# Kernel optimization log

Measured on AMD Instinct MI355X. Metric: run time of the kernel, lower is better.

Reference implementation:

```python
import jax, jax.numpy as jnp
import numpy as np

D_MODEL, D_STATE, EXPAND = 1024, 16, 2
D_INNER = EXPAND * D_MODEL
BATCH, SEQ = 4, 4096


def setup_inputs() -> dict:
    key = jax.random.key(0)
    ks = jax.random.split(key, 9)
    s = 0.02
    return {
        "x": jax.random.normal(ks[0], (BATCH, SEQ, D_MODEL), jnp.float32),
        # torch Linear weight [out,in] stored transposed here as [in,out]
        "W_in": jax.random.normal(ks[1], (D_MODEL, 2 * D_INNER), jnp.float32) * s,
        "conv_w": jax.random.normal(ks[2], (D_INNER, 1, 3), jnp.float32) * s,  # depthwise, groups=D_INNER
        "conv_b": jax.random.normal(ks[3], (D_INNER,), jnp.float32) * s,
        "W_B": jax.random.normal(ks[4], (D_INNER, D_STATE), jnp.float32) * s,
        "W_C": jax.random.normal(ks[5], (D_INNER, D_STATE), jnp.float32) * s,
        "A": jax.random.normal(ks[6], (D_STATE,), jnp.float32),
        "D": jnp.ones((D_INNER,), jnp.float32),
        "W_out": jax.random.normal(ks[7], (D_INNER, D_MODEL), jnp.float32) * s,
    }


def reference(x, W_in, conv_w, conv_b, W_B, W_C, A, D, W_out):
    d_inner = conv_w.shape[0]
    # input projection and split into main / residual gate paths
    xr = jnp.einsum("bld,de->ble", x, W_in)  # [B, L, 2*d_inner]
    x_main, res = xr[..., :d_inner], xr[..., d_inner:]
    # depthwise conv1d along seq (kernel 3, pad 1)
    xc = jax.lax.conv_general_dilated(
        x_main.transpose(0, 2, 1), conv_w, (1,), [(1, 1)],
        dimension_numbers=("NCH", "OIH", "NCH"), feature_group_count=d_inner)
    xc = (xc + conv_b[None, :, None]).transpose(0, 2, 1)  # [B, L, d_inner]
    xc = jax.nn.silu(xc)
    # selective-scan inputs
    Bt = jnp.einsum("bli,is->bls", xc, W_B)  # [B, L, d_state]
    Ct = jnp.einsum("bli,is->bls", xc, W_C)
    decay = jnp.exp(-jax.nn.softplus(A))  # exp(A_diag), [d_state]

    def step(state, bc):
        b_t, c_t = bc
        state = state * decay + b_t  # i=0: zeros*decay + B[0] == B[0]
        return state, jnp.sum(state * c_t, axis=-1)  # scalar per batch

    _, ys = jax.lax.scan(step, jnp.zeros_like(Bt[:, 0]),
                         (Bt.transpose(1, 0, 2), Ct.transpose(1, 0, 2)))
    ys = ys.T  # [B, L]
    y = ys[..., None] + xc * D  # broadcast scan output across d_inner
    y = y * jax.nn.silu(res)
    return jnp.einsum("bli,id->bld", y, W_out)
```

## Files before the change

### kernel.cpp

```cpp
#include <hip/hip_runtime.h>


typedef _Float16 half8 __attribute__((ext_vector_type(8)));
typedef float floatx4 __attribute__((ext_vector_type(4)));

#define D_MODEL 1024
#define D_INNER 2048
#define SEQ     4096
#define NBATCH  4
#define NROWS   (NBATCH * SEQ)
#define CHUNK   16
#define NCHUNK  (SEQ / CHUNK)
#define NTASK   (NBATCH * NCHUNK)

__device__ __forceinline__ void async16(_Float16* lds, const _Float16* g) {
    __builtin_amdgcn_global_load_lds((const __attribute__((address_space(1))) void*)g,
                                     (__attribute__((address_space(3))) void*)lds, 16, 0, 0);
}

__device__ __forceinline__ float siluf(float x) {
    return x / (1.f + __expf(-x));
}

__device__ __forceinline__ float decay_of(const float* A, int s) {
    return __expf(-log1pf(__expf(A[s])));
}


__global__ __launch_bounds__(256) void convert_f32_f16(const float* __restrict__ src,
                                                       _Float16* __restrict__ dst) {
    size_t idx = ((size_t)blockIdx.x * 256 + threadIdx.x) * 8;
    float4 a = *(const float4*)(src + idx);
    float4 b = *(const float4*)(src + idx + 4);
    half8 o = {(_Float16)a.x, (_Float16)a.y, (_Float16)a.z, (_Float16)a.w,
               (_Float16)b.x, (_Float16)b.y, (_Float16)b.z, (_Float16)b.w};
    *(half8*)(dst + idx) = o;
}

__global__ __launch_bounds__(256) void transpose_to_f16(const float* __restrict__ src,
                                                        _Float16* __restrict__ dst,
                                                        int K, int N) {
    __shared__ float tile[32][33];
    int n0 = blockIdx.x * 32, k0 = blockIdx.y * 32;
    int x = threadIdx.x, y = threadIdx.y;
#pragma unroll
    for (int r = 0; r < 32; r += 8)
        tile[y + r][x] = src[(size_t)(k0 + y + r) * N + (n0 + x)];
    __syncthreads();
#pragma unroll
    for (int r = 0; r < 32; r += 8)
        dst[(size_t)(n0 + y + r) * K + (k0 + x)] = (_Float16)tile[x][y + r];
}

__global__ __launch_bounds__(256) void convert_wbct(const float* __restrict__ WB,
                                                    const float* __restrict__ WC,
                                                    _Float16* __restrict__ WBCT) {
    int idx = blockIdx.x * 256 + threadIdx.x;
    int n = idx >> 11, k = idx & 2047;
    float v = (n < 16) ? WB[k * 16 + n] : WC[k * 16 + (n - 16)];
    WBCT[idx] = (_Float16)v;
}


__device__ __forceinline__ void stage_half(const _Float16* __restrict__ src, int K,
                                           int rowBase, int k0, _Float16* ldsHalf) {
    const int tid = threadIdx.x;
    const int sr = tid >> 3, wid = tid >> 6;
    const int lc = ((tid & 7) ^ (sr & 7)) << 3;
#pragma unroll
    for (int r = 0; r < 2; r++) {
        const _Float16* g = src + (size_t)(rowBase + r * 64 + sr) * K + (k0 + lc);
        async16(ldsHalf + r * 4096 + wid * 512, g);
    }
}

#define GP_LOAD(MQ, NQ, LOADA)                                                          \
    if (LOADA) {                                                                        \
        _Pragma("unroll") for (int m = 0; m < 4; m++) {                                 \
            const int lr = (MQ) * 128 + wm * 64 + m * 16 + fr;                          \
            _Pragma("unroll") for (int s = 0; s < 2; s++)                               \
                af[m][s] = *(const half8*)(Ab + lr * 64 + ((((s << 2) + q) ^ frq) << 3)); \
        }                                                                               \
    }                                                                                   \
    {                                                                                   \
        _Pragma("unroll") for (int n = 0; n < 2; n++) {                                 \
            const int br = (NQ) * 128 + wn * 32 + n * 16 + fr;                          \
            _Pragma("unroll") for (int s = 0; s < 2; s++)                               \
                bf[n][s] = *(const half8*)(Bb + br * 64 + ((((s << 2) + q) ^ frq) << 3)); \
        }                                                                               \
    }

#define GP_MMA(MQ, NQ)                                                                  \
    __builtin_amdgcn_s_barrier();                                                       \
    asm volatile("s_waitcnt lgkmcnt(0)" ::: "memory");                                  \
    __builtin_amdgcn_s_setprio(1);                                                      \
    _Pragma("unroll") for (int m = 0; m < 4; m++)                                       \
        _Pragma("unroll") for (int n = 0; n < 2; n++)                                   \
            _Pragma("unroll") for (int s = 0; s < 2; s++)                               \
                acc[(MQ) * 4 + m][(NQ) * 2 + n] = __builtin_amdgcn_mfma_f32_16x16x32_f16( \
                    af[m][s], bf[n][s], acc[(MQ) * 4 + m][(NQ) * 2 + n], 0, 0, 0);      \
    __builtin_amdgcn_s_setprio(0);                                                      \
    __builtin_amdgcn_s_barrier();

template <typename OutT>
__global__ __launch_bounds__(512, 2) void gemm256(const _Float16* __restrict__ A,
                                                  const _Float16* __restrict__ BT,
                                                  OutT* __restrict__ C,
                                                  int M, int N, int K) {
    __shared__ __align__(16) _Float16 smem[4 * 16384];
    _Float16* const AsBase = smem;
    _Float16* const BsBase = smem + 32768;

    const int tid = threadIdx.x;
    const int wid = tid >> 6, lane = tid & 63;
    const int wm = wid >> 2, wn = wid & 3;
    const int fr = lane & 15, q = lane >> 4, frq = fr & 7;

    int lin = blockIdx.y * gridDim.x + blockIdx.x;
    const int nwg = gridDim.x * gridDim.y;
    lin = (lin & 7) * (nwg >> 3) + (lin >> 3);
    const int bx = lin % gridDim.x, by = lin / gridDim.x;
    const int row0 = by * 256, col0 = bx * 256;
    const int NT = K >> 6;

    floatx4 acc[8][4] = {};
    half8 af[4][2], bf[2][2];

    stage_half(A,  K, row0,       0, AsBase);
    stage_half(BT, K, col0,       0, BsBase);
    stage_half(A,  K, row0 + 128, 0, AsBase + 8192);
    stage_half(BT, K, col0 + 128, 0, BsBase + 8192);
    if (NT > 1) {
        stage_half(A,  K, row0, 64, AsBase + 16384);
        stage_half(BT, K, col0, 64, BsBase + 16384);
        asm volatile("s_waitcnt vmcnt(4)" ::: "memory");
    } else {
        asm volatile("s_waitcnt vmcnt(0)" ::: "memory");
    }
    __builtin_amdgcn_s_barrier();

    for (int t = 0; t < NT; ++t) {
        _Float16* Ab  = AsBase + ((t & 1) << 14);
        _Float16* Bb  = BsBase + ((t & 1) << 14);
        _Float16* Abn = AsBase + (((t + 1) & 1) << 14);
        _Float16* Bbn = BsBase + (((t + 1) & 1) << 14);
        const int k1 = (t + 1) << 6, k2 = (t + 2) << 6;
        const bool s1 = (t + 1) < NT, s2 = (t + 2) < NT;

        GP_LOAD(0, 0, 1);
        if (s1) stage_half(A, K, row0 + 128, k1, Abn + 8192);
        GP_MMA(0, 0);

        GP_LOAD(0, 1, 0);
        if (s1) stage_half(BT, K, col0 + 128, k1, Bbn + 8192);
        GP_MMA(0, 1);

        GP_LOAD(1, 0, 1);
        if (s2) stage_half(A, K, row0, k2, Ab);
        GP_MMA(1, 0);

        GP_LOAD(1, 1, 0);
        if (s2) stage_half(BT, K, col0, k2, Bb);
        if (s2) {
            asm volatile("s_waitcnt vmcnt(4)" ::: "memory");
        } else if (t + 2 == NT) {
            asm volatile("s_waitcnt vmcnt(0)" ::: "memory");
        }
        GP_MMA(1, 1);
    }

    const int er = (lane >> 4) * 4, ec = lane & 15;
#pragma unroll
    for (int fi = 0; fi < 8; fi++)
#pragma unroll
        for (int fj = 0; fj < 4; fj++)
#pragma unroll
            for (int r = 0; r < 4; r++) {
                int row = row0 + (fi >> 2) * 128 + wm * 64 + (fi & 3) * 16 + er + r;
                int col = col0 + (fj >> 1) * 128 + wn * 32 + (fj & 1) * 16 + ec;
                C[(size_t)row * N + col] = (OutT)acc[fi][fj][r];
            }
}

__global__ __launch_bounds__(256) void conv_bc_fin(const _Float16* __restrict__ xr,
                                                   const float* __restrict__ cw,
                                                   const float* __restrict__ cb,
                                                   const _Float16* __restrict__ WBCT,
                                                   const float* __restrict__ A,
                                                   _Float16* __restrict__ xc,
                                                   float* __restrict__ BtCt,
                                                   float* __restrict__ fin) {
    __shared__ __align__(16) _Float16 As[4 * 32 * 128];
    const int tid = threadIdx.x, wid = tid >> 6, lane = tid & 63;
    const int row0 = blockIdx.x * 32;
    const int l0 = row0 & (SEQ - 1);
    const int cg = lane & 15;
    const int rg = lane >> 4;
    const int fr = lane & 15, q = lane >> 4;
    _Float16* As_w = As + wid * 4096;
    const int r0 = rg * 8;

    floatx4 acc[2][2] = {};

    for (int t = 0; t < 4; t++) {
        const int kbase = wid * 512 + t * 128;
        const int gcol = kbase + cg * 8;
        float w0[8], w1[8], w2[8], bb[8];
#pragma unroll
        for (int j = 0; j < 8; j++) {
            w0[j] = cw[(gcol + j) * 3];
            w1[j] = cw[(gcol + j) * 3 + 1];
            w2[j] = cw[(gcol + j) * 3 + 2];
            bb[j] = cb[gcol + j];
        }
        half8 prev = {}, cur, nxt;
        if (!(l0 == 0 && rg == 0))
            prev = *(const half8*)(xr + (size_t)(row0 + r0 - 1) * 4096 + gcol);
        cur = *(const half8*)(xr + (size_t)(row0 + r0) * 4096 + gcol);
#pragma unroll
        for (int r = 0; r < 8; r++) {
            if (r == 7 && rg == 3 && l0 + 32 == SEQ) {
                half8 z = {};
                nxt = z;
            } else {
                nxt = *(const half8*)(xr + (size_t)(row0 + r0 + r + 1) * 4096 + gcol);
            }
            half8 o;
#pragma unroll
            for (int j = 0; j < 8; j++) {
                float a = (float)prev[j] * w0[j] + (float)cur[j] * w1[j] +
                          (float)nxt[j] * w2[j] + bb[j];
                o[j] = (_Float16)siluf(a);
            }
            const int lrow = r0 + r;
            *(half8*)(xc + (size_t)(row0 + lrow) * D_INNER + gcol) = o;
            *(half8*)(As_w + lrow * 128 + ((cg ^ (lrow & 7)) * 8)) = o;
            prev = cur;
            cur = nxt;
        }
#pragma unroll
        for (int ks = 0; ks < 4; ks++) {
            half8 af[2], bf[2];
#pragma unroll
            for (int rt = 0; rt < 2; rt++)
                af[rt] = *(const half8*)(As_w + (rt * 16 + fr) * 128 +
                                         (((ks * 4 + q) ^ (fr & 7)) * 8));
#pragma unroll
            for (int ot = 0; ot < 2; ot++)
                bf[ot] = *(const half8*)(WBCT + (size_t)(ot * 16 + fr) * D_INNER +
                                         kbase + ks * 32 + q * 8);
#pragma unroll
            for (int rt = 0; rt < 2; rt++)
#pragma unroll
                for (int ot = 0; ot < 2; ot++)
                    acc[rt][ot] = __builtin_amdgcn_mfma_f32_16x16x32_f16(af[rt], bf[ot], acc[rt][ot], 0, 0, 0);
        }
    }

    __syncthreads();
    float* red = (float*)As;
    float* btl = (float*)As + 4096;
    const int er = (lane >> 4) * 4, ec = lane & 15;
#pragma unroll
    for (int rt = 0; rt < 2; rt++)
#pragma unroll
        for (int ot = 0; ot < 2; ot++)
#pragma unroll
            for (int rr = 0; rr < 4; rr++)
                red[wid * 1024 + (rt * 16 + er + rr) * 32 + ot * 16 + ec] = acc[rt][ot][rr];
    __syncthreads();
#pragma unroll
    for (int i = 0; i < 4; i++) {
        int idx = i * 256 + tid;
        float v = red[idx] + red[1024 + idx] + red[2048 + idx] + red[3072 + idx];
        btl[idx] = v;
        BtCt[(size_t)row0 * 32 + idx] = v;
    }
    __syncthreads();
    if (tid < 32) {
        const int ch = tid >> 4, s = tid & 15;
        const float decay = decay_of(A, s);
        float st = 0.f;
#pragma unroll
        for (int r = 0; r < CHUNK; r++)
            st = st * decay + btl[(ch * 16 + r) * 32 + s];
        fin[((row0 >> 4) + ch) * 16 + s] = st;
    }
}

__global__ __launch_bounds__(64) void scan_p2(const float* __restrict__ fin,
                                              const float* __restrict__ A,
                                              float* __restrict__ carry) {
    int t = threadIdx.x;
    int b = t >> 4, s = t & 15;
    float decay = decay_of(A, s);
    float d16 = decay;
#pragma unroll
    for (int k = 0; k < 4; k++) d16 *= d16;
    float cy = 0.f;
#pragma unroll 8
    for (int c = 0; c < NCHUNK; c++) {
        int idx = ((b * NCHUNK) + c) * 16 + s;
        carry[idx] = cy;
        cy = cy * d16 + fin[idx];
    }
}

__global__ __launch_bounds__(256) void scan_p3_fuse(const float* __restrict__ BtCt,
                                                    const float* __restrict__ A,
                                                    const float* __restrict__ carry,
                                                    const float* __restrict__ D,
                                                    const _Float16* __restrict__ xr,
                                                    _Float16* __restrict__ xc) {
    __shared__ float ysl[CHUNK];
    const int task = blockIdx.x;
    const int b = task >> 8, c = task & (NCHUNK - 1);
    const int row0 = b * SEQ + c * CHUNK;
    const int tid = threadIdx.x;

    if (tid < 16) {
        const int s = tid;
        const float decay = decay_of(A, s);
        size_t r = (size_t)row0 * 32;
        float bt[CHUNK], ct[CHUNK];
#pragma unroll
        for (int j = 0; j < CHUNK; j++) {
            bt[j] = BtCt[r + (size_t)j * 32 + s];
            ct[j] = BtCt[r + (size_t)j * 32 + 16 + s];
        }
        float st = carry[task * 16 + s];
        float yv[CHUNK];
#pragma unroll
        for (int j = 0; j < CHUNK; j++) {
            st = st * decay + bt[j];
            yv[j] = st * ct[j];
        }
#pragma unroll
        for (int j = 0; j < CHUNK; j++) {
            float y = yv[j];
            y += __shfl_xor(y, 1, 16);
            y += __shfl_xor(y, 2, 16);
            y += __shfl_xor(y, 4, 16);
            y += __shfl_xor(y, 8, 16);
            if (s == 0) ysl[j] = y;
        }
    }
    __syncthreads();

#pragma unroll
    for (int it = 0; it < 16; it++) {
        int chunk = it * 256 + tid;
        int rl = chunk >> 8;
        int colb = (chunk & 255) * 8;
        size_t row = (size_t)(row0 + rl);
        float yv = ysl[rl];
        half8 x8 = *(const half8*)(xc + row * D_INNER + colb);
        half8 r8 = *(const half8*)(xr + row * 4096 + 2048 + colb);
        float4 d0 = *(const float4*)(D + colb);
        float4 d1 = *(const float4*)(D + colb + 4);
        half8 o;
        float dd[8] = {d0.x, d0.y, d0.z, d0.w, d1.x, d1.y, d1.z, d1.w};
#pragma unroll
        for (int j = 0; j < 8; j++) {
            float y = yv + (float)x8[j] * dd[j];
            o[j] = (_Float16)(y * siluf((float)r8[j]));
        }
        *(half8*)(xc + row * D_INNER + colb) = o;
    }
}

extern "C" void kernel_launch(void* const* d_in, const int* in_sizes, int n_in,
                              void* d_out, int out_size, void* d_ws, size_t ws_size,
                              hipStream_t stream) {
    const float* x      = (const float*)d_in[0];
    const float* W_in   = (const float*)d_in[1];
    const float* conv_w = (const float*)d_in[2];
    const float* conv_b = (const float*)d_in[3];
    const float* W_B    = (const float*)d_in[4];
    const float* W_C    = (const float*)d_in[5];
    const float* A      = (const float*)d_in[6];
    const float* D      = (const float*)d_in[7];
    const float* W_out  = (const float*)d_in[8];
    float* out = (float*)d_out;

    char* ws = (char*)d_ws;
    size_t off = 0;
    auto alloc = [&](size_t bytes) { size_t o = off; off += (bytes + 255) & ~(size_t)255; return o; };
    _Float16* xh    = (_Float16*)(ws + alloc((size_t)NROWS * D_MODEL * 2));
    _Float16* WinT  = (_Float16*)(ws + alloc((size_t)4096 * 1024 * 2));
    _Float16* WoutT = (_Float16*)(ws + alloc((size_t)1024 * 2048 * 2));
    _Float16* WBCT  = (_Float16*)(ws + alloc((size_t)32 * 2048 * 2));
    _Float16* xr    = (_Float16*)(ws + alloc((size_t)NROWS * 4096 * 2));
    _Float16* xc    = (_Float16*)(ws + alloc((size_t)NROWS * D_INNER * 2));
    float*    BtCt  = (float*)(ws + alloc((size_t)NROWS * 32 * 4));
    float*    fin   = (float*)(ws + alloc((size_t)NTASK * 16 * 4));
    float*    carry = (float*)(ws + alloc((size_t)NTASK * 16 * 4));

    convert_f32_f16<<<(NROWS * D_MODEL) / (256 * 8), 256, 0, stream>>>(x, xh);
    transpose_to_f16<<<dim3(4096 / 32, 1024 / 32), dim3(32, 8), 0, stream>>>(W_in, WinT, 1024, 4096);
    transpose_to_f16<<<dim3(1024 / 32, 2048 / 32), dim3(32, 8), 0, stream>>>(W_out, WoutT, 2048, 1024);
    convert_wbct<<<(32 * 2048) / 256, 256, 0, stream>>>(W_B, W_C, WBCT);
    gemm256<_Float16><<<dim3(4096 / 256, NROWS / 256), 512, 0, stream>>>(xh, WinT, xr, NROWS, 4096, 1024);
    conv_bc_fin<<<NROWS / 32, 256, 0, stream>>>(xr, conv_w, conv_b, WBCT, A, xc, BtCt, fin);
    scan_p2<<<1, 64, 0, stream>>>(fin, A, carry);
    scan_p3_fuse<<<NTASK, 256, 0, stream>>>(BtCt, A, carry, D, xr, xc);
    gemm256<float><<<dim3(1024 / 256, NROWS / 256), 512, 0, stream>>>(xc, WoutT, out, NROWS, 1024, 2048);
}
```

Baseline: 450.0 us.

## Double-buffer B fragments in registers and drop explicit LDS waits in GEMM loop

```diff
diff --git a/kernel.cpp b/kernel.cpp
--- a/kernel.cpp
+++ b/kernel.cpp
@@ -74,31 +74,34 @@
     }
 }
 
-#define GP_LOAD(MQ, NQ, LOADA)                                                          \
-    if (LOADA) {                                                                        \
-        _Pragma("unroll") for (int m = 0; m < 4; m++) {                                 \
-            const int lr = (MQ) * 128 + wm * 64 + m * 16 + fr;                          \
-            _Pragma("unroll") for (int s = 0; s < 2; s++)                               \
-                af[m][s] = *(const half8*)(Ab + lr * 64 + ((((s << 2) + q) ^ frq) << 3)); \
-        }                                                                               \
-    }                                                                                   \
-    {                                                                                   \
-        _Pragma("unroll") for (int n = 0; n < 2; n++) {                                 \
-            const int br = (NQ) * 128 + wn * 32 + n * 16 + fr;                          \
-            _Pragma("unroll") for (int s = 0; s < 2; s++)                               \
-                bf[n][s] = *(const half8*)(Bb + br * 64 + ((((s << 2) + q) ^ frq) << 3)); \
-        }                                                                               \
-    }
-
-#define GP_MMA(MQ, NQ)                                                                  \
+__device__ __forceinline__ void loadA8(half8 af[4][2], const _Float16* Ab, int base,
+                                       int sw0, int sw1) {
+#pragma unroll
+    for (int m = 0; m < 4; m++) {
+        const _Float16* p = Ab + base + m * 1024;
+        af[m][0] = *(const half8*)(p + sw0);
+        af[m][1] = *(const half8*)(p + sw1);
+    }
+}
+
+__device__ __forceinline__ void loadB4(half8 bf[2][2], const _Float16* Bb, int base,
+                                       int sw0, int sw1) {
+#pragma unroll
+    for (int n = 0; n < 2; n++) {
+        const _Float16* p = Bb + base + n * 1024;
+        bf[n][0] = *(const half8*)(p + sw0);
+        bf[n][1] = *(const half8*)(p + sw1);
+    }
+}
+
+#define GP_MMA(MQ, NQ, BF)                                                              \
     __builtin_amdgcn_s_barrier();                                                       \
-    asm volatile("s_waitcnt lgkmcnt(0)" ::: "memory");                                  \
     __builtin_amdgcn_s_setprio(1);                                                      \
     _Pragma("unroll") for (int m = 0; m < 4; m++)                                       \
         _Pragma("unroll") for (int n = 0; n < 2; n++)                                   \
             _Pragma("unroll") for (int s = 0; s < 2; s++)                               \
                 acc[(MQ) * 4 + m][(NQ) * 2 + n] = __builtin_amdgcn_mfma_f32_16x16x32_f16( \
-                    af[m][s], bf[n][s], acc[(MQ) * 4 + m][(NQ) * 2 + n], 0, 0, 0);      \
+                    af[m][s], (BF)[n][s], acc[(MQ) * 4 + m][(NQ) * 2 + n], 0, 0, 0);    \
     __builtin_amdgcn_s_setprio(0);                                                      \
     __builtin_amdgcn_s_barrier();
 
@@ -115,6 +118,10 @@
     const int wid = tid >> 6, lane = tid & 63;
     const int wm = wid >> 2, wn = wid & 3;
     const int fr = lane & 15, q = lane >> 4, frq = fr & 7;
+    const int sw0 = (q ^ frq) << 3;
+    const int sw1 = ((4 + q) ^ frq) << 3;
+    const int aB0 = (wm * 64 + fr) * 64;
+    const int bB0 = (wn * 32 + fr) * 64;
 
     int lin = blockIdx.y * gridDim.x + blockIdx.x;
     const int nwg = gridDim.x * gridDim.y;
@@ -124,7 +131,7 @@
     const int NT = K >> 6;
 
     floatx4 acc[8][4] = {};
-    half8 af[4][2], bf[2][2];
+    half8 af[4][2], bf0[2][2], bf1[2][2];
 
     stage_half(A,  K, row0,       0, AsBase);
     stage_half(BT, K, col0,       0, BsBase);
@@ -138,6 +145,7 @@
         asm volatile("s_waitcnt vmcnt(0)" ::: "memory");
     }
     __builtin_amdgcn_s_barrier();
+    loadB4(bf0, BsBase, bB0, sw0, sw1);
 
     for (int t = 0; t < NT; ++t) {
         _Float16* Ab  = AsBase + ((t & 1) << 14);
@@ -147,26 +155,27 @@
         const int k1 = (t + 1) << 6, k2 = (t + 2) << 6;
         const bool s1 = (t + 1) < NT, s2 = (t + 2) < NT;
 
-        GP_LOAD(0, 0, 1);
+        loadA8(af, Ab, aB0, sw0, sw1);
+        loadB4(bf1, Bb, bB0 + 8192, sw0, sw1);
         if (s1) stage_half(A, K, row0 + 128, k1, Abn + 8192);
-        GP_MMA(0, 0);
-
-        GP_LOAD(0, 1, 0);
+        GP_MMA(0, 0, bf0);
+
         if (s1) stage_half(BT, K, col0 + 128, k1, Bbn + 8192);
-        GP_MMA(0, 1);
-
-        GP_LOAD(1, 0, 1);
+        GP_MMA(0, 1, bf1);
+
+        loadA8(af, Ab, aB0 + 8192, sw0, sw1);
         if (s2) stage_half(A, K, row0, k2, Ab);
-        GP_MMA(1, 0);
-
-        GP_LOAD(1, 1, 0);
+        GP_MMA(1, 0, bf0);
+
         if (s2) stage_half(BT, K, col0, k2, Bb);
         if (s2) {
             asm volatile("s_waitcnt vmcnt(4)" ::: "memory");
         } else if (t + 2 == NT) {
             asm volatile("s_waitcnt vmcnt(0)" ::: "memory");
         }
-        GP_MMA(1, 1);
+        __builtin_amdgcn_s_barrier();
+        loadB4(bf0, Bbn, bB0, sw0, sw1);
+        GP_MMA(1, 1, bf1);
     }
 
     const int er = (lane >> 4) * 4, ec = lane & 15;
```

Result: faster. 437.0 us (-2.9%).
